# Kernel optimization log

Measured on AMD Instinct MI355X. Metric: run time of the kernel, lower is better.

## Reference

```python
import jax, jax.numpy as jnp
import numpy as np

NUM_HIDDENS = 512
NUM_HEADS = 4
B, S = 4, 2048


def setup_inputs() -> dict:
    key = jax.random.key(0)
    ks = jax.random.split(key, 10)
    H = NUM_HIDDENS
    scale = 1.0 / np.sqrt(H)
    return {
        "queries": jax.random.normal(ks[0], (B, S, H), jnp.float32),
        "keys": jax.random.normal(ks[1], (B, S, H), jnp.float32),
        "values": jax.random.normal(ks[2], (B, S, H), jnp.float32),
        "attention_mask": jax.random.randint(ks[3], (B, S), 0, 2).astype(bool),
        "Wq": jax.random.normal(ks[4], (H, H), jnp.float32) * scale,
        "bq": jnp.zeros((H,), jnp.float32),
        "Wk": jax.random.normal(ks[5], (H, H), jnp.float32) * scale,
        "bk": jnp.zeros((H,), jnp.float32),
        "Wv": jax.random.normal(ks[6], (H, H), jnp.float32) * scale,
        "bv": jnp.zeros((H,), jnp.float32),
    }


def reference(queries, keys, values, attention_mask, Wq, bq, Wk, bk, Wv, bv):
    B_, S_, H = queries.shape
    nh = NUM_HEADS
    dh = H // nh

    # QKV projections with ReLU (as in the original Sequential(Linear, ReLU))
    q = jax.nn.relu(jnp.einsum("bsh,oh->bso", queries, Wq) + bq)
    k = jax.nn.relu(jnp.einsum("bsh,oh->bso", keys, Wk) + bk)
    v = jax.nn.relu(jnp.einsum("bsh,oh->bso", values, Wv) + bv)

    # chunk along last dim + stack dim=1  ==  reshape [B,S,nh,dh] -> [B,nh,S,dh]
    qs = q.reshape(B_, S_, nh, dh).transpose(0, 2, 1, 3)
    ks_ = k.reshape(B_, S_, nh, dh).transpose(0, 2, 1, 3)
    vs = v.reshape(B_, S_, nh, dh).transpose(0, 2, 1, 3)

    # scores [B, nh, S, S]
    score = jnp.einsum("bhqd,bhkd->bhqk", qs, ks_) / jnp.sqrt(jnp.float32(dh))

    # 'enc' mask: [B,S] -> [B,1,S,1], fills entire QUERY rows (faithful quirk)
    row_mask = attention_mask[:, None, :, None]
    score = jnp.where(row_mask, jnp.float32(-1e9), score)

    attn = jax.nn.softmax(score, axis=-1)
    a = jnp.einsum("bhqk,bhkd->bhqd", attn, vs)  # [B, nh, S, dh]

    # faithful quirk: permute(0,1,3,2) then reshape to (B, S, H)
    a = jnp.transpose(a, (0, 1, 3, 2)).reshape(B_, S_, H)
    return a + queries
```

## Files before the change

### kernel.cpp

```cpp
#include <hip/hip_runtime.h>
#include <hip/hip_bf16.h>

typedef __attribute__((ext_vector_type(8)))  __bf16 bf16x8;
typedef __attribute__((ext_vector_type(4)))  __bf16 bf16x4;
typedef __attribute__((ext_vector_type(2)))  __bf16 bf16x2;
typedef __attribute__((ext_vector_type(4)))  float  f32x4;
typedef __attribute__((ext_vector_type(16))) float  f32x16;

#define MFMA16(a,b,c) __builtin_amdgcn_mfma_f32_16x16x32_bf16((a),(b),(c),0,0,0)
#define MFMA32(a,b,c) __builtin_amdgcn_mfma_f32_32x32x16_bf16((a),(b),(c),0,0,0)

__device__ inline void gload_lds16(const __bf16* g, __bf16* l) {
  __builtin_amdgcn_global_load_lds(
      (const __attribute__((address_space(1))) void*)g,
      (__attribute__((address_space(3))) void*)l, 16, 0, 0);
}

__global__ __launch_bounds__(256, 2) void gemm_kernel(
    const float* __restrict__ Xq, const float* __restrict__ Xk,
    const float* __restrict__ Xv, const float* __restrict__ Wq,
    const float* __restrict__ Wk, const float* __restrict__ Wv,
    const float* __restrict__ bq, const float* __restrict__ bk,
    const float* __restrict__ bv, const int* __restrict__ mask,
    __bf16* __restrict__ dq, __bf16* __restrict__ dk, __bf16* __restrict__ dv)
{
  const int which = blockIdx.z;
  const float* X    = which == 0 ? Xq : which == 1 ? Xk : Xv;
  const float* W    = which == 0 ? Wq : which == 1 ? Wk : Wv;
  const float* bias = which == 0 ? bq : which == 1 ? bk : bv;
  __bf16* dst       = which == 0 ? dq : which == 1 ? dk : dv;
  const float oscale = which == 0 ? 0.12751744710339033f : 1.0f;

  __shared__ __align__(16) __bf16 Al[2][128 * 64];
  __shared__ __align__(16) __bf16 Bl[2][128 * 64];

  const int tid  = threadIdx.x;
  const int lane = tid & 63;
  const int w    = tid >> 6;
  const int wr = w >> 1, wc = w & 1;
  const int mbase = blockIdx.x * 128;
  const int nbase = blockIdx.y * 128;
  const int arow = lane & 15;
  const int hi   = lane >> 4;

  f32x4 acc[4][4] = {};
  float4 ar[8], br[8];

  auto issue = [&](int k0) {
#pragma unroll
    for (int i = 0; i < 8; ++i) {
      int idx = tid + i * 256;
      int r = idx >> 4, c = (idx & 15) * 4;
      ar[i] = *(const float4*)&X[(size_t)(mbase + r) * 512 + k0 + c];
      br[i] = *(const float4*)&W[(size_t)(nbase + r) * 512 + k0 + c];
    }
  };
  auto commit = [&](int buf) {
#pragma unroll
    for (int i = 0; i < 8; ++i) {
      int idx = tid + i * 256;
      int r = idx >> 4, c4 = idx & 15;
      int slot = c4 >> 1, half = c4 & 1;
      int addr = r * 64 + (slot ^ (r & 7)) * 8 + half * 4;
      bf16x4 av, bv2;
      av[0] = (__bf16)ar[i].x; av[1] = (__bf16)ar[i].y;
      av[2] = (__bf16)ar[i].z; av[3] = (__bf16)ar[i].w;
      bv2[0] = (__bf16)br[i].x; bv2[1] = (__bf16)br[i].y;
      bv2[2] = (__bf16)br[i].z; bv2[3] = (__bf16)br[i].w;
      *(bf16x4*)&Al[buf][addr] = av;
      *(bf16x4*)&Bl[buf][addr] = bv2;
    }
  };

  issue(0);
  commit(0);

  for (int t = 0; t < 8; ++t) {
    const int cur = t & 1;
    if (t < 7) issue((t + 1) * 64);
    __syncthreads();

    __builtin_amdgcn_s_setprio(1);
#pragma unroll
    for (int kk = 0; kk < 2; ++kk) {
      bf16x8 af[4], bfr[4];
#pragma unroll
      for (int m = 0; m < 4; ++m) {
        int row = wr * 64 + m * 16 + arow;
        int sl  = ((kk * 4 + hi) ^ (row & 7)) * 8;
        af[m] = *(bf16x8*)&Al[cur][row * 64 + sl];
      }
#pragma unroll
      for (int n = 0; n < 4; ++n) {
        int row = wc * 64 + n * 16 + arow;
        int sl  = ((kk * 4 + hi) ^ (row & 7)) * 8;
        bfr[n] = *(bf16x8*)&Bl[cur][row * 64 + sl];
      }
#pragma unroll
      for (int m = 0; m < 4; ++m)
#pragma unroll
        for (int n = 0; n < 4; ++n)
          acc[m][n] = MFMA16(af[m], bfr[n], acc[m][n]);
    }
    __builtin_amdgcn_s_setprio(0);

    if (t < 7) commit(cur ^ 1);
  }

#pragma unroll
  for (int n = 0; n < 4; ++n) {
    int col = nbase + wc * 64 + n * 16 + arow;
    float bsv = bias[col];
    int h = col >> 7, d = col & 127;
#pragma unroll
    for (int m = 0; m < 4; ++m) {
      int row0 = mbase + wr * 64 + m * 16 + hi * 4;
#pragma unroll
      for (int r = 0; r < 4; ++r) {
        float v = acc[m][n][r] + bsv;
        v = (v > 0.0f ? v : 0.0f) * oscale;
        int mm = row0 + r;
        int b = mm >> 11, s = mm & 2047;
        if (which == 0 && mask[b * 2048 + s] != 0) v = 0.0f;
        size_t bhoff = (size_t)(b * 4 + h) * (2048 * 128);
        if (which != 2) {
          dst[bhoff + (size_t)s * 128 + d] = (__bf16)v;
        } else {
          int tt = s >> 6, kw_ = (s >> 5) & 1, s2 = (s >> 4) & 1;
          int hi3 = (s >> 3) & 1, j = s & 7;
          int dblk = d >> 5, r5 = d & 31;
          size_t unit = (((size_t)tt * 2 + kw_) * 4 + dblk) * 2 + s2;
          dst[bhoff + unit * 512 + hi3 * 256 + r5 * 8 + j] = (__bf16)v;
        }
      }
    }
  }
}

__global__ __launch_bounds__(256, 2) void attn_kernel(
    const __bf16* __restrict__ qh, const __bf16* __restrict__ kh,
    const __bf16* __restrict__ vt, const float* __restrict__ queries,
    float* __restrict__ out)
{
  __shared__ __align__(16) __bf16 Kl[2][64 * 128];
  __shared__ float Mbuf[64 + 128 * 68];

  const int tid  = threadIdx.x;
  const int lane = tid & 63;
  const int w    = tid >> 6;
  const int qw   = w & 1;
  const int kw   = w >> 1;
  const int r5   = lane & 31;
  const int hi32 = lane >> 5;

  const int blk = blockIdx.x;
  const int xcd = blk & 7;
  const int idx = blk >> 3;
  const int bh  = xcd * 2 + (idx & 1);
  const int qt  = idx >> 1;
  const int b = bh >> 2, h = bh & 3;
  const int qbase = qt * 64 + qw * 32;

  const __bf16* qptr = qh + (size_t)bh * 2048 * 128;
  const __bf16* kptr = kh + (size_t)bh * 2048 * 128;
  const __bf16* vptr = vt + (size_t)bh * 2048 * 128;

  bf16x8 qf[8];
#pragma unroll
  for (int ds = 0; ds < 8; ++ds)
    qf[ds] = *(const bf16x8*)&qptr[(size_t)(qbase + r5) * 128 + ds * 16 + hi32 * 8];

  float l_st = 0.f;
  f32x16 oacc[4] = {};

  auto stageK = [&](int buf, int kv0) {
#pragma unroll
    for (int i = 0; i < 4; ++i) {
      int ob = i * 4096 + w * 1024;
      int o  = ob + lane * 16;
      int r  = o >> 8;
      int s  = ((o >> 4) & 15) ^ (r & 7);
      gload_lds16(kptr + (size_t)(kv0 + r) * 128 + s * 8, &Kl[buf][ob >> 1]);
    }
  };

  stageK(0, 0);

  for (int t = 0; t < 32; ++t) {
    const int cur = t & 1;

    bf16x8 vf[4][2];
#pragma unroll
    for (int dblk = 0; dblk < 4; ++dblk)
#pragma unroll
      for (int s = 0; s < 2; ++s)
        vf[dblk][s] = *(const bf16x8*)
            &vptr[((((size_t)t * 2 + kw) * 4 + dblk) * 2 + s) * 512 + lane * 8];
    asm volatile("" ::: "memory");
    __builtin_amdgcn_sched_barrier(0);

    if (t < 31) {
      stageK(cur ^ 1, (t + 1) * 64);
      asm volatile("s_waitcnt vmcnt(4)" ::: "memory");
    } else {
      asm volatile("s_waitcnt vmcnt(0)" ::: "memory");
    }
    __builtin_amdgcn_s_barrier();

    f32x16 sacc = {};
    __builtin_amdgcn_s_setprio(1);
#pragma unroll
    for (int ds = 0; ds < 8; ++ds) {
      int row = kw * 32 + r5;
      int sl  = ((ds * 2 + hi32) ^ (row & 7)) * 8;
      bf16x8 kf = *(bf16x8*)&Kl[cur][row * 128 + sl];
      sacc = MFMA32(kf, qf[ds], sacc);
    }
    __builtin_amdgcn_s_setprio(0);

    float ps[16];
#pragma unroll
    for (int r = 0; r < 16; ++r) {
      ps[r] = __builtin_amdgcn_exp2f(sacc[r]);
      sacc[r] = ps[r];
    }
#pragma unroll
    for (int st = 1; st < 16; st <<= 1)
#pragma unroll
      for (int r = 0; r < 16; r += 2 * st)
        ps[r] += ps[r + st];
    l_st += ps[0];

    unsigned pk[8];
#pragma unroll
    for (int g = 0; g < 8; ++g) {
      bf16x2 tp;
      tp[0] = (__bf16)sacc[2 * g];
      tp[1] = (__bf16)sacc[2 * g + 1];
      pk[g] = __builtin_bit_cast(unsigned, tp);
    }
    bf16x8 pf[2];
#pragma unroll
    for (int s = 0; s < 2; ++s) {
      unsigned a0 = pk[4 * s + 0], a1 = pk[4 * s + 1];
      unsigned b0 = pk[4 * s + 2], b1 = pk[4 * s + 3];
      asm("v_permlane32_swap_b32 %0, %1" : "+v"(a0), "+v"(b0));
      asm("v_permlane32_swap_b32 %0, %1" : "+v"(a1), "+v"(b1));
      union { unsigned u[4]; bf16x8 v; } pu;
      pu.u[0] = a0; pu.u[1] = a1; pu.u[2] = b0; pu.u[3] = b1;
      pf[s] = pu.v;
    }

    __builtin_amdgcn_s_setprio(1);
#pragma unroll
    for (int dblk = 0; dblk < 4; ++dblk)
#pragma unroll
      for (int s = 0; s < 2; ++s)
        oacc[dblk] = MFMA32(vf[dblk][s], pf[s], oacc[dblk]);
    __builtin_amdgcn_s_setprio(0);

    __builtin_amdgcn_s_barrier();
  }

  float l_tot = l_st + __shfl_xor(l_st, 32);

  __syncthreads();
  float* Ll = Mbuf;
  float* Ob = Mbuf + 64;

  if (kw == 1) {
    if (hi32 == 0) Ll[qw * 32 + r5] = l_tot;
    float* dst = Ob + (size_t)(qw * 64 + lane) * 68;
#pragma unroll
    for (int dblk = 0; dblk < 4; ++dblk)
      *(f32x16*)(dst + dblk * 16) = oacc[dblk];
  }
  __syncthreads();

  if (kw == 0) {
    float l1 = Ll[qw * 32 + r5];
    float inv = 1.0f / (l_tot + l1);
    const float* src = Ob + (size_t)(qw * 64 + lane) * 68;

    const int qhi = qt >> 3;
    const int col = (qt & 7) * 64 + qw * 32 + r5;
#pragma unroll
    for (int dblk = 0; dblk < 4; ++dblk) {
      f32x16 o1 = *(const f32x16*)(src + dblk * 16);
#pragma unroll
      for (int r = 0; r < 16; ++r) {
        int d = dblk * 32 + (r & 3) + 8 * (r >> 2) + 4 * hi32;
        int srow = h * 512 + d * 4 + qhi;
        size_t o = ((size_t)b * 2048 + srow) * 512 + col;
        out[o] = (oacc[dblk][r] + o1[r]) * inv + queries[o];
      }
    }
  }
}

extern "C" void kernel_launch(void* const* d_in, const int* in_sizes, int n_in,
                              void* d_out, int out_size, void* d_ws, size_t ws_size,
                              hipStream_t stream) {
  const float* queries = (const float*)d_in[0];
  const float* keys    = (const float*)d_in[1];
  const float* values  = (const float*)d_in[2];
  const int*   mask    = (const int*)d_in[3];
  const float* Wq = (const float*)d_in[4];
  const float* bq = (const float*)d_in[5];
  const float* Wk = (const float*)d_in[6];
  const float* bk = (const float*)d_in[7];
  const float* Wv = (const float*)d_in[8];
  const float* bv = (const float*)d_in[9];
  float* out = (float*)d_out;

  const size_t perX = (size_t)8192 * 512;
  __bf16* qhp = (__bf16*)d_ws;
  __bf16* khp = qhp + perX;
  __bf16* vtp = khp + perX;

  gemm_kernel<<<dim3(64, 4, 3), dim3(256), 0, stream>>>(
      queries, keys, values, Wq, Wk, Wv, bq, bk, bv, mask, qhp, khp, vtp);

  attn_kernel<<<dim3(512), dim3(256), 0, stream>>>(qhp, khp, vtp, queries, out);
}
```

Before: 80.92 us.

## Load K and V fragments directly to registers, drop LDS staging and barriers

The GEMM now writes K in a pre-fragmented MFMA layout, like V already is, so the attention kernel loads K fragments straight from global into registers. LDS double-buffering and the per-iteration block barriers go away. The attention block shrinks to two waves covering one 32-query tile, with twice as many blocks launched. K is prefetched one step ahead and V two steps ahead through ping-pong register buffers. In exchange, K is no longer shared across query waves through LDS, so global/L2 traffic for K doubles and register pressure rises.

```diff
diff --git a/kernel.cpp b/kernel.cpp
--- a/kernel.cpp
+++ b/kernel.cpp
@@ -123,13 +123,18 @@
         int b = mm >> 11, s = mm & 2047;
         if (which == 0 && mask[b * 2048 + s] != 0) v = 0.0f;
         size_t bhoff = (size_t)(b * 4 + h) * (2048 * 128);
-        if (which != 2) {
+        int tt = s >> 6, kw_ = (s >> 5) & 1;
+        if (which == 0) {
           dst[bhoff + (size_t)s * 128 + d] = (__bf16)v;
+        } else if (which == 1) {
+          int r5k = s & 31;
+          int ds = d >> 4, hi3 = (d >> 3) & 1, j = d & 7;
+          size_t unit = ((size_t)tt * 2 + kw_) * 8 + ds;
+          dst[bhoff + unit * 512 + hi3 * 256 + r5k * 8 + j] = (__bf16)v;
         } else {
-          int tt = s >> 6, kw_ = (s >> 5) & 1, s2 = (s >> 4) & 1;
-          int hi3 = (s >> 3) & 1, j = s & 7;
+          int s2 = (s >> 4) & 1, hi3 = (s >> 3) & 1, j = s & 7;
           int dblk = d >> 5, r5 = d & 31;
-          size_t unit = (((size_t)tt * 2 + kw_) * 4 + dblk) * 2 + s2;
+          size_t unit = ((size_t)tt * 2 + kw_) * 8 + dblk * 2 + s2;
           dst[bhoff + unit * 512 + hi3 * 256 + r5 * 8 + j] = (__bf16)v;
         }
       }
@@ -137,33 +142,31 @@
   }
 }
 
-__global__ __launch_bounds__(256, 2) void attn_kernel(
-    const __bf16* __restrict__ qh, const __bf16* __restrict__ kh,
-    const __bf16* __restrict__ vt, const float* __restrict__ queries,
+__global__ __launch_bounds__(128, 2) void attn_kernel(
+    const __bf16* __restrict__ qh, const __bf16* __restrict__ kfr,
+    const __bf16* __restrict__ vfr, const float* __restrict__ queries,
     float* __restrict__ out)
 {
-  __shared__ __align__(16) __bf16 Kl[2][64 * 128];
-  __shared__ float Mbuf[64 + 128 * 68];
+  __shared__ float Ll[32];
+  __shared__ __align__(16) float Ob[64 * 68];
 
   const int tid  = threadIdx.x;
   const int lane = tid & 63;
-  const int w    = tid >> 6;
-  const int qw   = w & 1;
-  const int kw   = w >> 1;
+  const int kw   = tid >> 6;
   const int r5   = lane & 31;
   const int hi32 = lane >> 5;
 
-  const int blk = blockIdx.x;
-  const int xcd = blk & 7;
-  const int idx = blk >> 3;
-  const int bh  = xcd * 2 + (idx & 1);
-  const int qt  = idx >> 1;
+  const int blk  = blockIdx.x;
+  const int xcd  = blk & 7;
+  const int rest = blk >> 3;
+  const int bh   = xcd * 2 + (rest & 1);
+  const int qt   = rest >> 1;
   const int b = bh >> 2, h = bh & 3;
-  const int qbase = qt * 64 + qw * 32;
-
-  const __bf16* qptr = qh + (size_t)bh * 2048 * 128;
-  const __bf16* kptr = kh + (size_t)bh * 2048 * 128;
-  const __bf16* vptr = vt + (size_t)bh * 2048 * 128;
+  const int qbase = qt * 32;
+
+  const __bf16* qptr = qh  + (size_t)bh * 2048 * 128;
+  const __bf16* kp   = kfr + (size_t)bh * 2048 * 128;
+  const __bf16* vp   = vfr + (size_t)bh * 2048 * 128;
 
   bf16x8 qf[8];
 #pragma unroll
@@ -172,51 +175,30 @@
 
   float l_st = 0.f;
   f32x16 oacc[4] = {};
-
-  auto stageK = [&](int buf, int kv0) {
-#pragma unroll
-    for (int i = 0; i < 4; ++i) {
-      int ob = i * 4096 + w * 1024;
-      int o  = ob + lane * 16;
-      int r  = o >> 8;
-      int s  = ((o >> 4) & 15) ^ (r & 7);
-      gload_lds16(kptr + (size_t)(kv0 + r) * 128 + s * 8, &Kl[buf][ob >> 1]);
-    }
-  };
-
-  stageK(0, 0);
-
-  for (int t = 0; t < 32; ++t) {
-    const int cur = t & 1;
-
-    bf16x8 vf[4][2];
-#pragma unroll
-    for (int dblk = 0; dblk < 4; ++dblk)
-#pragma unroll
-      for (int s = 0; s < 2; ++s)
-        vf[dblk][s] = *(const bf16x8*)
-            &vptr[((((size_t)t * 2 + kw) * 4 + dblk) * 2 + s) * 512 + lane * 8];
-    asm volatile("" ::: "memory");
-    __builtin_amdgcn_sched_barrier(0);
-
-    if (t < 31) {
-      stageK(cur ^ 1, (t + 1) * 64);
-      asm volatile("s_waitcnt vmcnt(4)" ::: "memory");
-    } else {
-      asm volatile("s_waitcnt vmcnt(0)" ::: "memory");
-    }
-    __builtin_amdgcn_s_barrier();
-
+  bf16x8 kf[8], vfA[8], vfB[8];
+
+  auto loadK = [&](int t) {
+#pragma unroll
+    for (int ds = 0; ds < 8; ++ds)
+      kf[ds] = *(const bf16x8*)
+          &kp[(((size_t)t * 2 + kw) * 8 + ds) * 512 + lane * 8];
+  };
+  auto loadV = [&](bf16x8 (&dstv)[8], int t) {
+#pragma unroll
+    for (int u = 0; u < 8; ++u)
+      dstv[u] = *(const bf16x8*)
+          &vp[(((size_t)t * 2 + kw) * 8 + u) * 512 + lane * 8];
+  };
+
+  auto body = [&](int t, bf16x8 (&vcur)[8]) {
     f32x16 sacc = {};
     __builtin_amdgcn_s_setprio(1);
 #pragma unroll
-    for (int ds = 0; ds < 8; ++ds) {
-      int row = kw * 32 + r5;
-      int sl  = ((ds * 2 + hi32) ^ (row & 7)) * 8;
-      bf16x8 kf = *(bf16x8*)&Kl[cur][row * 128 + sl];
-      sacc = MFMA32(kf, qf[ds], sacc);
-    }
+    for (int ds = 0; ds < 8; ++ds)
+      sacc = MFMA32(kf[ds], qf[ds], sacc);
     __builtin_amdgcn_s_setprio(0);
+
+    if (t + 1 < 32) loadK(t + 1);
 
     float ps[16];
 #pragma unroll
@@ -253,37 +235,40 @@
 
     __builtin_amdgcn_s_setprio(1);
 #pragma unroll
+    for (int u = 0; u < 8; ++u)
+      oacc[u >> 1] = MFMA32(vcur[u], pf[u & 1], oacc[u >> 1]);
+    __builtin_amdgcn_s_setprio(0);
+
+    if (t + 2 < 32) loadV(vcur, t + 2);
+  };
+
+  loadK(0);
+  loadV(vfA, 0);
+  loadV(vfB, 1);
+
+  for (int tt = 0; tt < 16; ++tt) {
+    body(2 * tt, vfA);
+    body(2 * tt + 1, vfB);
+  }
+
+  float l_tot = l_st + __shfl_xor(l_st, 32);
+
+  if (kw == 1) {
+    if (hi32 == 0) Ll[r5] = l_tot;
+    float* dstp = Ob + (size_t)lane * 68;
+#pragma unroll
     for (int dblk = 0; dblk < 4; ++dblk)
-#pragma unroll
-      for (int s = 0; s < 2; ++s)
-        oacc[dblk] = MFMA32(vf[dblk][s], pf[s], oacc[dblk]);
-    __builtin_amdgcn_s_setprio(0);
-
-    __builtin_amdgcn_s_barrier();
-  }
-
-  float l_tot = l_st + __shfl_xor(l_st, 32);
-
+      *(f32x16*)(dstp + dblk * 16) = oacc[dblk];
+  }
   __syncthreads();
-  float* Ll = Mbuf;
-  float* Ob = Mbuf + 64;
-
-  if (kw == 1) {
-    if (hi32 == 0) Ll[qw * 32 + r5] = l_tot;
-    float* dst = Ob + (size_t)(qw * 64 + lane) * 68;
-#pragma unroll
-    for (int dblk = 0; dblk < 4; ++dblk)
-      *(f32x16*)(dst + dblk * 16) = oacc[dblk];
-  }
-  __syncthreads();
 
   if (kw == 0) {
-    float l1 = Ll[qw * 32 + r5];
+    float l1 = Ll[r5];
     float inv = 1.0f / (l_tot + l1);
-    const float* src = Ob + (size_t)(qw * 64 + lane) * 68;
-
-    const int qhi = qt >> 3;
-    const int col = (qt & 7) * 64 + qw * 32 + r5;
+    const float* src = Ob + (size_t)lane * 68;
+
+    const int qhi = qt >> 4;
+    const int col = (qt & 15) * 32 + r5;
 #pragma unroll
     for (int dblk = 0; dblk < 4; ++dblk) {
       f32x16 o1 = *(const f32x16*)(src + dblk * 16);
@@ -321,5 +306,5 @@
   gemm_kernel<<<dim3(64, 4, 3), dim3(256), 0, stream>>>(
       queries, keys, values, Wq, Wk, Wv, bq, bk, bv, mask, qhp, khp, vtp);
 
-  attn_kernel<<<dim3(512), dim3(256), 0, stream>>>(qhp, khp, vtp, queries, out);
+  attn_kernel<<<dim3(1024), dim3(128), 0, stream>>>(qhp, khp, vtp, queries, out);
 }
```

After: 86.67 us. +7.1%, slower.
